# Performance work log

Measured on AMD Instinct MI355X. Metric: run time of the kernel, lower is better.

## Reference

```python
import jax, jax.numpy as jnp
import numpy as np

EMBED_DIM = 1024
NUM_HEADS = 16
FFN_DIM = 4096
N_QUBITS = 8
LN_EPS = 1e-5


def _layernorm(x, g, b):
    mu = jnp.mean(x, axis=-1, keepdims=True)
    var = jnp.mean(jnp.square(x - mu), axis=-1, keepdims=True)
    return (x - mu) * jax.lax.rsqrt(var + LN_EPS) * g + b


def setup_inputs() -> dict:
    key = jax.random.key(0)
    ks = jax.random.split(key, 12)
    E, F_, Q = EMBED_DIM, FFN_DIM, N_QUBITS
    s = 1.0 / np.sqrt(E)
    return {
        "x": jax.random.normal(ks[0], (4, 2048, E), dtype=jnp.float32),
        "wq": jax.random.normal(ks[1], (E, E), dtype=jnp.float32) * s,
        "wk": jax.random.normal(ks[2], (E, E), dtype=jnp.float32) * s,
        "wv": jax.random.normal(ks[3], (E, E), dtype=jnp.float32) * s,
        "wo": jax.random.normal(ks[4], (E, E), dtype=jnp.float32) * s,
        "theta": jax.random.normal(ks[5], (Q,), dtype=jnp.float32),
        "w1": jax.random.normal(ks[6], (Q, F_), dtype=jnp.float32) * (1.0 / np.sqrt(Q)),
        "w2": jax.random.normal(ks[7], (F_, E), dtype=jnp.float32) * (1.0 / np.sqrt(F_)),
        "ln1_g": jnp.ones((E,), dtype=jnp.float32),
        "ln1_b": jnp.zeros((E,), dtype=jnp.float32),
        "ln2_g": jnp.ones((E,), dtype=jnp.float32),
        "ln2_b": jnp.zeros((E,), dtype=jnp.float32),
    }


def reference(x, wq, wk, wv, wo, theta, w1, w2, ln1_g, ln1_b, ln2_g, ln2_b):
    B, S, E = x.shape
    H, Dk = NUM_HEADS, E // NUM_HEADS
    # ---- multi-head attention ----
    q = (x @ wq).reshape(B, S, H, Dk).transpose(0, 2, 1, 3)  # [B,H,S,Dk]
    k = (x @ wk).reshape(B, S, H, Dk).transpose(0, 2, 1, 3)
    v = (x @ wv).reshape(B, S, H, Dk).transpose(0, 2, 1, 3)
    scores = jnp.einsum("bhsd,bhtd->bhst", q, k) / np.sqrt(Dk)
    attn = jax.nn.softmax(scores, axis=-1)
    ctx = jnp.einsum("bhst,bhtd->bhsd", attn, v)
    ctx = ctx.transpose(0, 2, 1, 3).reshape(B, S, E)
    attn_out = ctx @ wo
    x1 = _layernorm(x + attn_out, ln1_g, ln1_b)
    # ---- quantum FFN ----
    # Per qubit w: |0> -> RX(x1_w) -> RX(x1_w) -> RX(theta_w); <Z> = cos(2*x1_w + theta_w)
    q_out = jnp.cos(2.0 * x1[..., :N_QUBITS] + theta)  # [B,S,Q]
    ffn_out = jax.nn.relu(q_out @ w1) @ w2  # [B,S,E]
    return _layernorm(x1 + ffn_out, ln2_g, ln2_b)
```

## Files before the change

### kernel.cpp

```cpp
#include <hip/hip_runtime.h>
#include <hip/hip_bf16.h>


typedef __attribute__((ext_vector_type(8))) short bf16x8;
typedef __attribute__((ext_vector_type(16))) float f32x16;
typedef __attribute__((ext_vector_type(4))) unsigned short u16x4;

__device__ __forceinline__ unsigned short f2bf(float f) {
  union { float f; unsigned int u; } v; v.f = f;
  return (unsigned short)((v.u + 0x7FFFu + ((v.u >> 16) & 1u)) >> 16);
}
__device__ __forceinline__ float bf2f(unsigned short h) {
  union { unsigned int u; float f; } v; v.u = ((unsigned int)h) << 16;
  return v.f;
}
__device__ __forceinline__ f32x16 mfma32(bf16x8 a, bf16x8 b, f32x16 c) {
  return __builtin_amdgcn_mfma_f32_32x32x16_bf16(a, b, c, 0, 0, 0);
}
__device__ __forceinline__ void lds_cp16(const void* g, void* l) {
  __builtin_amdgcn_global_load_lds(
      (const __attribute__((address_space(1))) unsigned int*)g,
      (__attribute__((address_space(3))) unsigned int*)l, 16, 0, 0);
}

#define QG_CONV(P, FC0, FC1)                                                  \
  {                                                                           \
    int x0a, x0b, x1a, x1b, x2a, x2b, x3a, x3b;                               \
    asm("v_cvt_pk_bf16_f32 %0, %1, %2" : "=v"(x0a) : "v"(P[0]),  "v"(P[1]));  \
    asm("v_cvt_pk_bf16_f32 %0, %1, %2" : "=v"(x0b) : "v"(P[2]),  "v"(P[3]));  \
    asm("v_cvt_pk_bf16_f32 %0, %1, %2" : "=v"(x1a) : "v"(P[4]),  "v"(P[5]));  \
    asm("v_cvt_pk_bf16_f32 %0, %1, %2" : "=v"(x1b) : "v"(P[6]),  "v"(P[7]));  \
    asm("v_cvt_pk_bf16_f32 %0, %1, %2" : "=v"(x2a) : "v"(P[8]),  "v"(P[9]));  \
    asm("v_cvt_pk_bf16_f32 %0, %1, %2" : "=v"(x2b) : "v"(P[10]), "v"(P[11])); \
    asm("v_cvt_pk_bf16_f32 %0, %1, %2" : "=v"(x3a) : "v"(P[12]), "v"(P[13])); \
    asm("v_cvt_pk_bf16_f32 %0, %1, %2" : "=v"(x3b) : "v"(P[14]), "v"(P[15])); \
    asm("v_permlane32_swap_b32 %0, %1" : "+v"(x0a), "+v"(x1a));               \
    asm("v_permlane32_swap_b32 %0, %1" : "+v"(x0b), "+v"(x1b));               \
    asm("v_permlane32_swap_b32 %0, %1" : "+v"(x2a), "+v"(x3a));               \
    asm("v_permlane32_swap_b32 %0, %1" : "+v"(x2b), "+v"(x3b));               \
    union { int u[4]; bf16x8 v; } f0_, f1_;                                   \
    f0_.u[0] = x0a; f0_.u[1] = x0b; f0_.u[2] = x1a; f0_.u[3] = x1b;           \
    f1_.u[0] = x2a; f1_.u[1] = x2b; f1_.u[2] = x3a; f1_.u[3] = x3b;           \
    FC0 = f0_.v; FC1 = f1_.v;                                                 \
  }

__global__ __launch_bounds__(256) void cast_x_kernel(const float* __restrict__ in,
                                                     unsigned short* __restrict__ out,
                                                     int n4) {
  int i = blockIdx.x * 256 + threadIdx.x;
  if (i >= n4) return;
  float4 v = ((const float4*)in)[i];
  u16x4 o = { f2bf(v.x), f2bf(v.y), f2bf(v.z), f2bf(v.w) };
  ((u16x4*)out)[i] = o;
}

__global__ __launch_bounds__(256) void prep_weights(const float* __restrict__ wq,
                                                    const float* __restrict__ wk,
                                                    const float* __restrict__ wv,
                                                    const float* __restrict__ wo,
                                                    const float* __restrict__ w2,
                                                    const float* __restrict__ w1,
                                                    unsigned short* __restrict__ wqkvT,
                                                    unsigned short* __restrict__ woT,
                                                    unsigned short* __restrict__ w2T,
                                                    unsigned short* __restrict__ w1t) {
  __shared__ float tile[32][33];
  const int tx = threadIdx.x, ty = threadIdx.y;
  const int z = blockIdx.z;

  if (z == 0 && blockIdx.y >= 32) {
    if (blockIdx.y < 48) {
      const int f = (blockIdx.y - 32) * 256 + ty * 32 + tx;
      unsigned short v[8];
#pragma unroll
      for (int q = 0; q < 8; q++) v[q] = f2bf(w1[q * 4096 + f]);
      *(u16x4*)(w1t + f * 8)     = (u16x4){v[0], v[1], v[2], v[3]};
      *(u16x4*)(w1t + f * 8 + 4) = (u16x4){v[4], v[5], v[6], v[7]};
    }
    return;
  }
  if (z < 4 && blockIdx.y >= 32) return;

  const float* src;
  unsigned short* dst;
  int K;
  if (z == 4)      { src = w2; dst = w2T; K = 4096; }
  else if (z == 0) { src = wq; dst = wqkvT; K = 1024; }
  else if (z == 1) { src = wk; dst = wqkvT + 1024 * 1024; K = 1024; }
  else if (z == 2) { src = wv; dst = wqkvT + 2048 * 1024; K = 1024; }
  else             { src = wo; dst = woT; K = 1024; }
  const int N = 1024;
  const int n0 = blockIdx.x * 32, k0 = blockIdx.y * 32;
#pragma unroll
  for (int i = 0; i < 32; i += 8)
    tile[ty + i][tx] = src[(long)(k0 + ty + i) * N + n0 + tx];
  __syncthreads();
#pragma unroll
  for (int i = 0; i < 32; i += 8)
    dst[(long)(n0 + ty + i) * K + k0 + tx] = f2bf(tile[tx][ty + i]);
}

__global__ __launch_bounds__(256) void vt_kernel(const unsigned short* __restrict__ qkv,
                                                 unsigned short* __restrict__ vT) {
  __shared__ unsigned short tile[32][34];
  const int t0 = blockIdx.x * 32, d0 = blockIdx.y * 32, bh = blockIdx.z;
  const int b = bh >> 4, h = bh & 15;
  const int tx = threadIdx.x, ty = threadIdx.y;
  const unsigned short* src = qkv + (long)(b * 2048 + t0) * 3072 + 2048 + h * 64 + d0;
#pragma unroll
  for (int i = 0; i < 32; i += 8)
    tile[ty + i][tx] = src[(long)(ty + i) * 3072 + tx];
  __syncthreads();
  unsigned short* dst = vT + ((long)bh * 64 + d0) * 2048 + t0;
#pragma unroll
  for (int i = 0; i < 32; i += 8)
    dst[(long)(ty + i) * 2048 + tx] = tile[tx][ty + i];
}

template<int EPI>
__global__ __launch_bounds__(256) void gemm_bt3(const unsigned short* __restrict__ A,
                                                const unsigned short* __restrict__ BT,
                                                void* __restrict__ Cv,
                                                int M, int N, int K) {
  __shared__ __align__(16) unsigned char smem[2][32768];
  const int tid = threadIdx.x;
  const int l = tid & 63, w = tid >> 6;
  const int l32 = l & 31, h32 = l >> 5;
  const int wrm = (w >> 1) * 64;
  const int wrn = (w & 1) * 64;

  const int nx = gridDim.x;
  const int nwg = nx * gridDim.y;
  const int orig = blockIdx.y * nx + blockIdx.x;
  const int chunk = nwg >> 3;
  const int logical = (orig & 7) * chunk + (orig >> 3);
  const long m0 = (long)(logical / nx) * 128;
  const long n0 = (long)(logical % nx) * 128;

  const unsigned short* gp[8];
  unsigned ldsoff[8];
#pragma unroll
  for (int i = 0; i < 8; i++) {
    const int c = (i & 3) * 256 + tid;
    const int r = c >> 3, k8 = c & 7;
    if (i < 4) {
      gp[i] = A + (m0 + r) * (long)K + (k8 ^ (r & 7)) * 8;
      ldsoff[i] = (unsigned)c * 16;
    } else {
      gp[i] = BT + (n0 + r) * (long)K + (k8 ^ (r & 7)) * 8;
      ldsoff[i] = 16384u + (unsigned)c * 16;
    }
  }

  f32x16 acc[2][2];
#pragma unroll
  for (int mf = 0; mf < 2; mf++)
#pragma unroll
    for (int nf = 0; nf < 2; nf++)
#pragma unroll
      for (int e = 0; e < 16; e++) acc[mf][nf][e] = 0.f;

  const int NT = K >> 6;
#define STAGE(bf, t)                                                    \
  do {                                                                  \
    unsigned char* _d = &smem[bf][0];                                   \
    const long _ko = (long)(t) * 64;                                    \
    _Pragma("unroll")                                                   \
    for (int _i = 0; _i < 8; _i++)                                      \
      lds_cp16(gp[_i] + _ko, _d + ldsoff[_i]);                          \
  } while (0)

  STAGE(0, 0);
  int cur = 0;
  for (int t = 0; t < NT; t++) {
    if (t + 1 < NT) {
      STAGE(cur ^ 1, t + 1);
      asm volatile("s_waitcnt vmcnt(8)" ::: "memory");
    } else {
      asm volatile("s_waitcnt vmcnt(0)" ::: "memory");
    }
    __builtin_amdgcn_sched_barrier(0);
    __builtin_amdgcn_s_barrier();
    __builtin_amdgcn_sched_barrier(0);

    const unsigned char* bufA = &smem[cur][0];
    const unsigned char* bufB = &smem[cur][16384];
    bf16x8 af[2][4], bfr[2][4];
#pragma unroll
    for (int mf = 0; mf < 2; mf++) {
      const int r = wrm + mf * 32 + l32;
#pragma unroll
      for (int ks = 0; ks < 4; ks++)
        af[mf][ks] = *(const bf16x8*)(bufA + r * 128 + (((ks * 2 + h32) ^ (r & 7)) * 16));
    }
#pragma unroll
    for (int nf = 0; nf < 2; nf++) {
      const int r = wrn + nf * 32 + l32;
#pragma unroll
      for (int ks = 0; ks < 4; ks++)
        bfr[nf][ks] = *(const bf16x8*)(bufB + r * 128 + (((ks * 2 + h32) ^ (r & 7)) * 16));
    }
    __builtin_amdgcn_s_setprio(1);
#pragma unroll
    for (int ks = 0; ks < 4; ks++)
#pragma unroll
      for (int mf = 0; mf < 2; mf++)
#pragma unroll
        for (int nf = 0; nf < 2; nf++)
          acc[mf][nf] = mfma32(af[mf][ks], bfr[nf][ks], acc[mf][nf]);
    __builtin_amdgcn_s_setprio(0);
    __builtin_amdgcn_sched_barrier(0);
    __builtin_amdgcn_s_barrier();
    cur ^= 1;
  }
#undef STAGE

#pragma unroll
  for (int mf = 0; mf < 2; mf++)
#pragma unroll
    for (int nf = 0; nf < 2; nf++) {
      const long c0 = n0 + wrn + nf * 32 + l32;
#pragma unroll
      for (int reg = 0; reg < 16; reg++) {
        const long r0 = m0 + wrm + mf * 32 + (reg & 3) + 8 * (reg >> 2) + 4 * h32;
        if (EPI == 0) ((float*)Cv)[r0 * (long)N + c0] = acc[mf][nf][reg];
        else ((unsigned short*)Cv)[r0 * (long)N + c0] = f2bf(acc[mf][nf][reg]);
      }
    }
}

__global__ __launch_bounds__(512) void ffn_fused(const unsigned short* __restrict__ qo,
                                                 const unsigned short* __restrict__ w1t,
                                                 const unsigned short* __restrict__ BT,
                                                 unsigned short* __restrict__ Cp0,
                                                 unsigned short* __restrict__ Cp1,
                                                 int N, int K) {
  __shared__ __align__(16) unsigned char sm[4 * 16384 + 32768 + 4096];
  unsigned char* lsW = sm + 65536;
  unsigned char* lsQ = sm + 98304;
  const int tid = threadIdx.x;
  const int l = tid & 63, w = tid >> 6;
  const int l32 = l & 31, h32 = l >> 5;
  const int wrm = (w >> 1) * 64;
  const int wrn = (w & 1) * 64;

  const int nx = gridDim.x;
  const int nwg = nx * gridDim.y;
  const int orig = blockIdx.y * nx + blockIdx.x;
  const int chunk = nwg >> 3;
  const int logical = (orig & 7) * chunk + (orig >> 3);
  const long m0 = (long)(logical / nx) * 256;
  const long n0 = (long)(logical % nx) * 256;
  const int kz = blockIdx.z;
  const int NT = (K >> 6) >> 1;
  const int tbase = kz * NT;
  unsigned short* C = kz ? Cp1 : Cp0;

  const unsigned short* gpB[2][2];
  unsigned offB[2];
#pragma unroll
  for (int i = 0; i < 2; i++) {
    const int c = i * 512 + tid;
    const int r = c >> 3, k8 = c & 7;
#pragma unroll
    for (int nt2 = 0; nt2 < 2; nt2++)
      gpB[nt2][i] = BT + (n0 + nt2 * 128 + r) * (long)K + (long)tbase * 64 + (k8 ^ (r & 7)) * 8;
    offB[i] = (unsigned)c * 16;
  }
  const unsigned short* w1base = w1t + (long)tbase * 64 * 8;

  const bf16x8 z8 = {0, 0, 0, 0, 0, 0, 0, 0};

#define STAGE_B(bf, t)                                                  \
  do {                                                                  \
    const long _ko = (long)(t) * 64;                                    \
    _Pragma("unroll")                                                   \
    for (int _n = 0; _n < 2; _n++) {                                    \
      unsigned char* _d = sm + ((bf) * 2 + _n) * 16384;                 \
      lds_cp16(gpB[_n][0] + _ko, _d + offB[0]);                         \
      lds_cp16(gpB[_n][1] + _ko, _d + offB[1]);                         \
    }                                                                   \
  } while (0)

#pragma unroll
  for (int i = 0; i < 4; i++) {
    const int slot = i * 8 + w;
    lds_cp16(w1base + (long)(slot * 64 + l) * 8, lsW + ((unsigned)slot << 10));
  }
  if (w < 4) lds_cp16(qo + (m0 + w * 64 + l) * 8, lsQ + (unsigned)(w * 64) * 16);
  STAGE_B(0, 0);
  asm volatile("s_waitcnt vmcnt(0)" ::: "memory");
  __builtin_amdgcn_s_barrier();

  bf16x8 qof[2];
#pragma unroll
  for (int mf = 0; mf < 2; mf++)
    qof[mf] = (h32 == 0) ? *(const bf16x8*)(lsQ + (wrm + mf * 32 + l32) * 16) : z8;

  f32x16 zz;
#pragma unroll
  for (int e = 0; e < 16; e++) zz[e] = 0.f;
  f32x16 acc[2][2][2];
#pragma unroll
  for (int nt2 = 0; nt2 < 2; nt2++)
#pragma unroll
    for (int mf = 0; mf < 2; mf++)
#pragma unroll
      for (int nf = 0; nf < 2; nf++) acc[nt2][mf][nf] = zz;

  int cur = 0;
  for (int t = 0; t < NT; t++) {
    if (t + 1 < NT) {
      STAGE_B(cur ^ 1, t + 1);
      asm volatile("s_waitcnt vmcnt(4)" ::: "memory");
    } else {
      asm volatile("s_waitcnt vmcnt(0)" ::: "memory");
    }
    __builtin_amdgcn_sched_barrier(0);
    __builtin_amdgcn_s_barrier();
    __builtin_amdgcn_sched_barrier(0);

    bf16x8 w1f[2];
#pragma unroll
    for (int tg = 0; tg < 2; tg++)
      w1f[tg] = (h32 == 0)
          ? *(const bf16x8*)(lsW + ((unsigned)t << 10) + (tg * 32 + l32) * 16) : z8;

    __builtin_amdgcn_s_setprio(1);
    f32x16 hC0 = mfma32(w1f[0], qof[0], zz);
    f32x16 hC1 = mfma32(w1f[1], qof[0], zz);
    f32x16 hD0 = mfma32(w1f[0], qof[1], zz);
    f32x16 hD1 = mfma32(w1f[1], qof[1], zz);
    __builtin_amdgcn_s_setprio(0);
#pragma unroll
    for (int e = 0; e < 16; e++) {
      hC0[e] = fmaxf(hC0[e], 0.f);
      hC1[e] = fmaxf(hC1[e], 0.f);
      hD0[e] = fmaxf(hD0[e], 0.f);
      hD1[e] = fmaxf(hD1[e], 0.f);
    }
    bf16x8 a0, a1, a2, a3, b0, b1, b2, b3;
    QG_CONV(hC0, a0, a1)
    QG_CONV(hC1, a2, a3)
    QG_CONV(hD0, b0, b1)
    QG_CONV(hD1, b2, b3)

#pragma unroll
    for (int nt2 = 0; nt2 < 2; nt2++) {
      const unsigned char* bufB = sm + (cur * 2 + nt2) * 16384;
      bf16x8 bfr[2][4];
#pragma unroll
      for (int nf = 0; nf < 2; nf++) {
        const int r = wrn + nf * 32 + l32;
#pragma unroll
        for (int ks = 0; ks < 4; ks++)
          bfr[nf][ks] = *(const bf16x8*)(bufB + r * 128 + (((ks * 2 + h32) ^ (r & 7)) * 16));
      }
      __builtin_amdgcn_s_setprio(1);
      acc[nt2][0][0] = mfma32(a0, bfr[0][0], acc[nt2][0][0]);
      acc[nt2][0][0] = mfma32(a1, bfr[0][1], acc[nt2][0][0]);
      acc[nt2][0][0] = mfma32(a2, bfr[0][2], acc[nt2][0][0]);
      acc[nt2][0][0] = mfma32(a3, bfr[0][3], acc[nt2][0][0]);
      acc[nt2][0][1] = mfma32(a0, bfr[1][0], acc[nt2][0][1]);
      acc[nt2][0][1] = mfma32(a1, bfr[1][1], acc[nt2][0][1]);
      acc[nt2][0][1] = mfma32(a2, bfr[1][2], acc[nt2][0][1]);
      acc[nt2][0][1] = mfma32(a3, bfr[1][3], acc[nt2][0][1]);
      acc[nt2][1][0] = mfma32(b0, bfr[0][0], acc[nt2][1][0]);
      acc[nt2][1][0] = mfma32(b1, bfr[0][1], acc[nt2][1][0]);
      acc[nt2][1][0] = mfma32(b2, bfr[0][2], acc[nt2][1][0]);
      acc[nt2][1][0] = mfma32(b3, bfr[0][3], acc[nt2][1][0]);
      acc[nt2][1][1] = mfma32(b0, bfr[1][0], acc[nt2][1][1]);
      acc[nt2][1][1] = mfma32(b1, bfr[1][1], acc[nt2][1][1]);
      acc[nt2][1][1] = mfma32(b2, bfr[1][2], acc[nt2][1][1]);
      acc[nt2][1][1] = mfma32(b3, bfr[1][3], acc[nt2][1][1]);
      __builtin_amdgcn_s_setprio(0);
    }

    __builtin_amdgcn_sched_barrier(0);
    __builtin_amdgcn_s_barrier();
    cur ^= 1;
  }
#undef STAGE_B

#pragma unroll
  for (int nt2 = 0; nt2 < 2; nt2++)
#pragma unroll
    for (int mf = 0; mf < 2; mf++)
#pragma unroll
      for (int nf = 0; nf < 2; nf++) {
        const long c0 = n0 + nt2 * 128 + wrn + nf * 32 + l32;
#pragma unroll
        for (int reg = 0; reg < 16; reg++) {
          const long r0 = m0 + wrm + mf * 32 + (reg & 3) + 8 * (reg >> 2) + 4 * h32;
          C[r0 * (long)N + c0] = f2bf(acc[nt2][mf][nf][reg]);
        }
      }
}

#define QG_BLOCK(P, LIP, FC0, FC1)                                            \
  {                                                                           \
    _Pragma("unroll")                                                         \
    for (int e = 0; e < 16; e++)                                              \
      asm("v_exp_f32 %0, %1" : "=v"(P[e]) : "v"(P[e]));                       \
    float s_ = 0.f;                                                           \
    _Pragma("unroll")                                                         \
    for (int e = 0; e < 16; e++) s_ += P[e];                                  \
    LIP += s_;                                                                \
    QG_CONV(P, FC0, FC1)                                                      \
  }

__global__ __launch_bounds__(256) void attn_kernel(const unsigned short* __restrict__ qkv,
                                                   const unsigned short* __restrict__ vT,
                                                   unsigned short* __restrict__ ctx) {
  __shared__ __align__(16) unsigned short lsK[64][72];
  __shared__ __align__(16) unsigned short lsV[64][72];

  const int tid = threadIdx.x;
  const int l = tid & 63, w = tid >> 6;
  const int l32 = l & 31, h32 = l >> 5;

  const int orig = blockIdx.x;
  const int logical = (orig & 7) * 64 + (orig >> 3);
  const int s0 = (logical & 7) * 256;
  const int bh = logical >> 3;
  const int b = bh >> 4, hh = bh & 15;

  const float QSC = 0.18033688f;
  const unsigned short* qg_base = qkv + (long)(b * 2048 + s0 + w * 64) * 3072 + hh * 64;
  bf16x8 qb0[4], qb1[4];
#pragma unroll
  for (int kc = 0; kc < 4; kc++) {
    bf16x8 t0v = *(const bf16x8*)(qg_base + (long)l32 * 3072 + kc * 16 + h32 * 8);
    bf16x8 t1v = *(const bf16x8*)(qg_base + (long)(32 + l32) * 3072 + kc * 16 + h32 * 8);
#pragma unroll
    for (int j = 0; j < 8; j++) {
      t0v[j] = (short)f2bf(bf2f((unsigned short)t0v[j]) * QSC);
      t1v[j] = (short)f2bf(bf2f((unsigned short)t1v[j]) * QSC);
    }
    qb0[kc] = t0v;
    qb1[kc] = t1v;
  }

  f32x16 oacc00, oacc01, oacc10, oacc11;
#pragma unroll
  for (int e = 0; e < 16; e++) {
    oacc00[e] = 0.f; oacc01[e] = 0.f; oacc10[e] = 0.f; oacc11[e] = 0.f;
  }
  float lip0 = 0.f, lip1 = 0.f;

  const int tr = tid >> 2;
  const int tc = (tid & 3) * 16;
  const unsigned short* kbase = qkv + (long)(b * 2048) * 3072 + 1024 + hh * 64;
  const unsigned short* vbase = vT + (long)bh * 64 * 2048;

  bf16x8 k0 = *(const bf16x8*)(kbase + (long)tr * 3072 + tc);
  bf16x8 k1 = *(const bf16x8*)(kbase + (long)tr * 3072 + tc + 8);
  bf16x8 v0 = *(const bf16x8*)(vbase + (long)tr * 2048 + tc);
  bf16x8 v1 = *(const bf16x8*)(vbase + (long)tr * 2048 + tc + 8);

  for (int t0 = 0; t0 < 2048; t0 += 64) {
    __syncthreads();
    *(bf16x8*)&lsK[tr][tc]     = k0;
    *(bf16x8*)&lsK[tr][tc + 8] = k1;
    *(bf16x8*)&lsV[tr][tc]     = v0;
    *(bf16x8*)&lsV[tr][tc + 8] = v1;
    __syncthreads();
    if (t0 + 64 < 2048) {
      k0 = *(const bf16x8*)(kbase + (long)(t0 + 64 + tr) * 3072 + tc);
      k1 = *(const bf16x8*)(kbase + (long)(t0 + 64 + tr) * 3072 + tc + 8);
      v0 = *(const bf16x8*)(vbase + (long)tr * 2048 + t0 + 64 + tc);
      v1 = *(const bf16x8*)(vbase + (long)tr * 2048 + t0 + 64 + tc + 8);
    }

#pragma unroll
    for (int tg = 0; tg < 2; tg++) {
      bf16x8 kb[4];
#pragma unroll
      for (int kc = 0; kc < 4; kc++)
        kb[kc] = *(const bf16x8*)&lsK[tg * 32 + l32][kc * 16 + h32 * 8];

      f32x16 p0, p1;
#pragma unroll
      for (int e = 0; e < 16; e++) { p0[e] = 0.f; p1[e] = 0.f; }
      __builtin_amdgcn_s_setprio(1);
#pragma unroll
      for (int kc = 0; kc < 4; kc++) {
        p0 = mfma32(kb[kc], qb0[kc], p0);
        p1 = mfma32(kb[kc], qb1[kc], p1);
      }
      __builtin_amdgcn_s_setprio(0);

      bf16x8 fA0, fA1, fB0, fB1;
      QG_BLOCK(p0, lip0, fA0, fA1)
      QG_BLOCK(p1, lip1, fB0, fB1)

      bf16x8 v00 = *(const bf16x8*)&lsV[l32][tg * 32 + h32 * 8];
      bf16x8 v01 = *(const bf16x8*)&lsV[l32][tg * 32 + 16 + h32 * 8];
      bf16x8 v10 = *(const bf16x8*)&lsV[32 + l32][tg * 32 + h32 * 8];
      bf16x8 v11 = *(const bf16x8*)&lsV[32 + l32][tg * 32 + 16 + h32 * 8];

      __builtin_amdgcn_s_setprio(1);
      oacc00 = mfma32(fA0, v00, oacc00);
      oacc00 = mfma32(fA1, v01, oacc00);
      oacc01 = mfma32(fA0, v10, oacc01);
      oacc01 = mfma32(fA1, v11, oacc01);
      oacc10 = mfma32(fB0, v00, oacc10);
      oacc10 = mfma32(fB1, v01, oacc10);
      oacc11 = mfma32(fB0, v10, oacc11);
      oacc11 = mfma32(fB1, v11, oacc11);
      __builtin_amdgcn_s_setprio(0);
    }
  }

  const float li0 = lip0 + __shfl_xor(lip0, 32);
  const float li1 = lip1 + __shfl_xor(lip1, 32);
  const float inv0 = 1.f / li0;
  const float inv1 = 1.f / li1;
  const long qrow0 = (long)(b * 2048 + s0 + w * 64);
  const int dcol = hh * 64 + l32;
#define STORE_QG(OA, OB, INV, QOFF)                                           \
  _Pragma("unroll")                                                           \
  for (int reg = 0; reg < 16; reg++) {                                        \
    const int rq = (reg & 3) + 8 * (reg >> 2) + 4 * h32;                      \
    const float iv = __shfl(INV, rq);                                         \
    const long q = qrow0 + (QOFF) + rq;                                       \
    ctx[q * 1024 + dcol]      = f2bf(OA[reg] * iv);                           \
    ctx[q * 1024 + dcol + 32] = f2bf(OB[reg] * iv);                           \
  }
  STORE_QG(oacc00, oacc01, inv0, 0)
  STORE_QG(oacc10, oacc11, inv1, 32)
#undef STORE_QG
}

__global__ __launch_bounds__(256) void ln1_kernel(const float* __restrict__ x,
                                                  const unsigned short* __restrict__ ao,
                                                  const float* __restrict__ g,
                                                  const float* __restrict__ bb,
                                                  unsigned short* __restrict__ x1,
                                                  unsigned short* __restrict__ qo,
                                                  const float* __restrict__ theta) {
  const int row = blockIdx.x;
  const int tid = threadIdx.x;
  const long base = (long)row * 1024 + tid * 4;
  float4 a = *(const float4*)(x + base);
  u16x4 o = *(const u16x4*)(ao + base);
  float4 r;
  r.x = a.x + bf2f(o[0]); r.y = a.y + bf2f(o[1]);
  r.z = a.z + bf2f(o[2]); r.w = a.w + bf2f(o[3]);
  float s  = r.x + r.y + r.z + r.w;
  float ss = r.x * r.x + r.y * r.y + r.z * r.z + r.w * r.w;
  for (int off = 32; off; off >>= 1) {
    s  += __shfl_down(s, off);
    ss += __shfl_down(ss, off);
  }
  __shared__ float red[4][2];
  const int wv = tid >> 6;
  if ((tid & 63) == 0) { red[wv][0] = s; red[wv][1] = ss; }
  __syncthreads();
  s  = red[0][0] + red[1][0] + red[2][0] + red[3][0];
  ss = red[0][1] + red[1][1] + red[2][1] + red[3][1];
  const float mu  = s * (1.f / 1024.f);
  const float var = ss * (1.f / 1024.f) - mu * mu;
  const float rsv = rsqrtf(var + 1e-5f);
  float4 gv  = *(const float4*)(g + tid * 4);
  float4 bbv = *(const float4*)(bb + tid * 4);
  float y0 = (r.x - mu) * rsv * gv.x + bbv.x;
  float y1 = (r.y - mu) * rsv * gv.y + bbv.y;
  float y2 = (r.z - mu) * rsv * gv.z + bbv.z;
  float y3 = (r.w - mu) * rsv * gv.w + bbv.w;
  *(u16x4*)(x1 + base) = (u16x4){f2bf(y0), f2bf(y1), f2bf(y2), f2bf(y3)};
  if (tid < 2) {
    float yv[4] = {y0, y1, y2, y3};
    u16x4 q;
#pragma unroll
    for (int c = 0; c < 4; c++)
      q[c] = f2bf(__cosf(2.f * yv[c] + theta[tid * 4 + c]));
    *(u16x4*)(qo + (long)row * 8 + tid * 4) = q;
  }
}

__global__ __launch_bounds__(256) void ln2_kernel(const unsigned short* __restrict__ x1,
                                                  const unsigned short* __restrict__ p0,
                                                  const unsigned short* __restrict__ p1,
                                                  const float* __restrict__ g,
                                                  const float* __restrict__ bb,
                                                  float* __restrict__ out) {
  const int row = blockIdx.x;
  const int tid = threadIdx.x;
  const long base = (long)row * 1024 + tid * 4;
  u16x4 a = *(const u16x4*)(x1 + base);
  u16x4 b = *(const u16x4*)(p0 + base);
  u16x4 c = *(const u16x4*)(p1 + base);
  float4 r;
  r.x = bf2f(a[0]) + bf2f(b[0]) + bf2f(c[0]);
  r.y = bf2f(a[1]) + bf2f(b[1]) + bf2f(c[1]);
  r.z = bf2f(a[2]) + bf2f(b[2]) + bf2f(c[2]);
  r.w = bf2f(a[3]) + bf2f(b[3]) + bf2f(c[3]);
  float s  = r.x + r.y + r.z + r.w;
  float ss = r.x * r.x + r.y * r.y + r.z * r.z + r.w * r.w;
  for (int off = 32; off; off >>= 1) {
    s  += __shfl_down(s, off);
    ss += __shfl_down(ss, off);
  }
  __shared__ float red[4][2];
  const int wv = tid >> 6;
  if ((tid & 63) == 0) { red[wv][0] = s; red[wv][1] = ss; }
  __syncthreads();
  s  = red[0][0] + red[1][0] + red[2][0] + red[3][0];
  ss = red[0][1] + red[1][1] + red[2][1] + red[3][1];
  const float mu  = s * (1.f / 1024.f);
  const float var = ss * (1.f / 1024.f) - mu * mu;
  const float rsv = rsqrtf(var + 1e-5f);
  float4 gv  = *(const float4*)(g + tid * 4);
  float4 bbv = *(const float4*)(bb + tid * 4);
  float4 y;
  y.x = (r.x - mu) * rsv * gv.x + bbv.x;
  y.y = (r.y - mu) * rsv * gv.y + bbv.y;
  y.z = (r.z - mu) * rsv * gv.z + bbv.z;
  y.w = (r.w - mu) * rsv * gv.w + bbv.w;
  *(float4*)(out + base) = y;
}

extern "C" void kernel_launch(void* const* d_in, const int* in_sizes, int n_in,
                              void* d_out, int out_size, void* d_ws, size_t ws_size,
                              hipStream_t stream) {
  const float* x     = (const float*)d_in[0];
  const float* wq    = (const float*)d_in[1];
  const float* wk    = (const float*)d_in[2];
  const float* wv    = (const float*)d_in[3];
  const float* wo    = (const float*)d_in[4];
  const float* theta = (const float*)d_in[5];
  const float* w1    = (const float*)d_in[6];
  const float* w2    = (const float*)d_in[7];
  const float* g1    = (const float*)d_in[8];
  const float* b1    = (const float*)d_in[9];
  const float* g2    = (const float*)d_in[10];
  const float* b2    = (const float*)d_in[11];
  float* out = (float*)d_out;
  char* ws = (char*)d_ws;

  const long MB = 1 << 20;
  unsigned short* xb    = (unsigned short*)(ws);
  unsigned short* wqkvT = (unsigned short*)(ws + 16 * MB);
  unsigned short* woT   = (unsigned short*)(ws + 22 * MB);
  unsigned short* w2T   = (unsigned short*)(ws + 24 * MB);
  unsigned short* x1b   = (unsigned short*)(ws + 32 * MB);
  unsigned short* aob   = (unsigned short*)(ws + 64 * MB);
  unsigned short* p0b   = aob;
  unsigned short* p1b   = (unsigned short*)(ws + 80 * MB);
  unsigned short* qkv   = (unsigned short*)(ws + 96 * MB);
  unsigned short* vTb   = (unsigned short*)(ws + 144 * MB);
  unsigned short* qob   = (unsigned short*)(ws + 160 * MB);
  unsigned short* w1tb  = (unsigned short*)(ws + 160 * MB + 128 * 1024);
  unsigned short* ctx   = xb;

  cast_x_kernel<<<8192, 256, 0, stream>>>(x, xb, 8192 * 1024 / 4);
  dim3 tb(32, 8);
  prep_weights<<<dim3(32, 128, 5), tb, 0, stream>>>(wq, wk, wv, wo, w2, w1,
                                                    wqkvT, woT, w2T, w1tb);

  gemm_bt3<1><<<dim3(24, 64), 256, 0, stream>>>(xb, wqkvT, qkv, 8192, 3072, 1024);

  vt_kernel<<<dim3(64, 2, 64), tb, 0, stream>>>(qkv, vTb);

  attn_kernel<<<512, 256, 0, stream>>>(qkv, vTb, ctx);

  gemm_bt3<1><<<dim3(8, 64), 256, 0, stream>>>(ctx, woT, aob, 8192, 1024, 1024);

  ln1_kernel<<<8192, 256, 0, stream>>>(x, aob, g1, b1, x1b, qob, theta);

  ffn_fused<<<dim3(4, 32, 2), 512, 0, stream>>>(qob, w1tb, w2T, p0b, p1b, 1024, 4096);

  ln2_kernel<<<8192, 256, 0, stream>>>(x1b, p0b, p1b, g2, b2, out);
}
```

Measured before the change: 293.5 us.

## Halve attention query tile per block to double grid size

The attention kernel now gives each wave 32 query rows instead of 64, so a block covers 128 queries and the grid grows from 512 to 1024 blocks. This raises parallelism and occupancy (fewer accumulator registers, more blocks across CUs) on a GPU with many CUs. In exchange, each block reloads the full K/V stream for half as many queries, which doubles K/V global and LDS traffic per unit of work and lowers MFMA reuse per LDS read.

```diff
diff --git a/kernel.cpp b/kernel.cpp
--- a/kernel.cpp
+++ b/kernel.cpp
@@ -420,33 +420,27 @@
   const int l32 = l & 31, h32 = l >> 5;
 
   const int orig = blockIdx.x;
-  const int logical = (orig & 7) * 64 + (orig >> 3);
-  const int s0 = (logical & 7) * 256;
-  const int bh = logical >> 3;
+  const int logical = (orig & 7) * 128 + (orig >> 3);
+  const int s0 = (logical & 15) * 128;
+  const int bh = logical >> 4;
   const int b = bh >> 4, hh = bh & 15;
 
   const float QSC = 0.18033688f;
-  const unsigned short* qg_base = qkv + (long)(b * 2048 + s0 + w * 64) * 3072 + hh * 64;
-  bf16x8 qb0[4], qb1[4];
+  const unsigned short* qg_base = qkv + (long)(b * 2048 + s0 + w * 32) * 3072 + hh * 64;
+  bf16x8 qb0[4];
 #pragma unroll
   for (int kc = 0; kc < 4; kc++) {
     bf16x8 t0v = *(const bf16x8*)(qg_base + (long)l32 * 3072 + kc * 16 + h32 * 8);
-    bf16x8 t1v = *(const bf16x8*)(qg_base + (long)(32 + l32) * 3072 + kc * 16 + h32 * 8);
-#pragma unroll
-    for (int j = 0; j < 8; j++) {
+#pragma unroll
+    for (int j = 0; j < 8; j++)
       t0v[j] = (short)f2bf(bf2f((unsigned short)t0v[j]) * QSC);
-      t1v[j] = (short)f2bf(bf2f((unsigned short)t1v[j]) * QSC);
-    }
     qb0[kc] = t0v;
-    qb1[kc] = t1v;
-  }
-
-  f32x16 oacc00, oacc01, oacc10, oacc11;
-#pragma unroll
-  for (int e = 0; e < 16; e++) {
-    oacc00[e] = 0.f; oacc01[e] = 0.f; oacc10[e] = 0.f; oacc11[e] = 0.f;
-  }
-  float lip0 = 0.f, lip1 = 0.f;
+  }
+
+  f32x16 oacc00, oacc01;
+#pragma unroll
+  for (int e = 0; e < 16; e++) { oacc00[e] = 0.f; oacc01[e] = 0.f; }
+  float lip0 = 0.f;
 
   const int tr = tid >> 2;
   const int tc = (tid & 3) * 16;
@@ -479,20 +473,17 @@
       for (int kc = 0; kc < 4; kc++)
         kb[kc] = *(const bf16x8*)&lsK[tg * 32 + l32][kc * 16 + h32 * 8];
 
-      f32x16 p0, p1;
-#pragma unroll
-      for (int e = 0; e < 16; e++) { p0[e] = 0.f; p1[e] = 0.f; }
+      f32x16 p0;
+#pragma unroll
+      for (int e = 0; e < 16; e++) p0[e] = 0.f;
       __builtin_amdgcn_s_setprio(1);
 #pragma unroll
-      for (int kc = 0; kc < 4; kc++) {
+      for (int kc = 0; kc < 4; kc++)
         p0 = mfma32(kb[kc], qb0[kc], p0);
-        p1 = mfma32(kb[kc], qb1[kc], p1);
-      }
       __builtin_amdgcn_s_setprio(0);
 
-      bf16x8 fA0, fA1, fB0, fB1;
+      bf16x8 fA0, fA1;
       QG_BLOCK(p0, lip0, fA0, fA1)
-      QG_BLOCK(p1, lip1, fB0, fB1)
 
       bf16x8 v00 = *(const bf16x8*)&lsV[l32][tg * 32 + h32 * 8];
       bf16x8 v01 = *(const bf16x8*)&lsV[l32][tg * 32 + 16 + h32 * 8];
@@ -504,32 +495,22 @@
       oacc00 = mfma32(fA1, v01, oacc00);
       oacc01 = mfma32(fA0, v10, oacc01);
       oacc01 = mfma32(fA1, v11, oacc01);
-      oacc10 = mfma32(fB0, v00, oacc10);
-      oacc10 = mfma32(fB1, v01, oacc10);
-      oacc11 = mfma32(fB0, v10, oacc11);
-      oacc11 = mfma32(fB1, v11, oacc11);
       __builtin_amdgcn_s_setprio(0);
     }
   }
 
   const float li0 = lip0 + __shfl_xor(lip0, 32);
-  const float li1 = lip1 + __shfl_xor(lip1, 32);
   const float inv0 = 1.f / li0;
-  const float inv1 = 1.f / li1;
-  const long qrow0 = (long)(b * 2048 + s0 + w * 64);
+  const long qrow0 = (long)(b * 2048 + s0 + w * 32);
   const int dcol = hh * 64 + l32;
-#define STORE_QG(OA, OB, INV, QOFF)                                           \
-  _Pragma("unroll")                                                           \
-  for (int reg = 0; reg < 16; reg++) {                                        \
-    const int rq = (reg & 3) + 8 * (reg >> 2) + 4 * h32;                      \
-    const float iv = __shfl(INV, rq);                                         \
-    const long q = qrow0 + (QOFF) + rq;                                       \
-    ctx[q * 1024 + dcol]      = f2bf(OA[reg] * iv);                           \
-    ctx[q * 1024 + dcol + 32] = f2bf(OB[reg] * iv);                           \
-  }
-  STORE_QG(oacc00, oacc01, inv0, 0)
-  STORE_QG(oacc10, oacc11, inv1, 32)
-#undef STORE_QG
+#pragma unroll
+  for (int reg = 0; reg < 16; reg++) {
+    const int rq = (reg & 3) + 8 * (reg >> 2) + 4 * h32;
+    const float iv = __shfl(inv0, rq);
+    const long q = qrow0 + rq;
+    ctx[q * 1024 + dcol]      = f2bf(oacc00[reg] * iv);
+    ctx[q * 1024 + dcol + 32] = f2bf(oacc01[reg] * iv);
+  }
 }
 
 __global__ __launch_bounds__(256) void ln1_kernel(const float* __restrict__ x,
@@ -663,7 +644,7 @@
 
   vt_kernel<<<dim3(64, 2, 64), tb, 0, stream>>>(qkv, vTb);
 
-  attn_kernel<<<512, 256, 0, stream>>>(qkv, vTb, ctx);
+  attn_kernel<<<1024, 256, 0, stream>>>(qkv, vTb, ctx);
 
   gemm_bt3<1><<<dim3(8, 64), 256, 0, stream>>>(ctx, woT, aob, 8192, 1024, 1024);
 
```

New measurement: 304.7 us. 3.8% more time.
